# Performance work log

Hardware: AMD Instinct MI355X
Metric: run time of the kernel (lower is better)

The kernel has to match this reference:

```python
import jax, jax.numpy as jnp
import numpy as np

V, T, K, L, D = 256, 256, 36, 32, 1024
TAU = 0.05
MODE = 0
NEG_INF = -jnp.inf


def setup_inputs() -> dict:
    key = jax.random.key(0)
    k1, k2 = jax.random.split(key)
    imgs = jax.random.normal(k1, (V, K, D), dtype=jnp.float32)
    caps = jax.random.normal(k2, (T, L, D), dtype=jnp.float32)
    # Full lengths: the original module writes -inf into sim and 0 into w at
    # padded positions, so padding would produce -inf*0 = NaN in the output.
    img_lens = jnp.full((V,), K, dtype=jnp.int32)
    cap_lens = jnp.full((T,), L, dtype=jnp.int32)
    return {"imgs": imgs, "caps": caps, "img_lens": img_lens, "cap_lens": cap_lens}


def _l2norm(x):
    return x / jnp.maximum(jnp.linalg.norm(x, axis=-1, keepdims=True), 1e-12)


def reference(imgs, caps, img_lens, cap_lens):
    # masks: [V,K], [T,L]
    img_mask = (jnp.arange(K)[None, :] < img_lens[:, None]).astype(imgs.dtype)
    cap_mask = (jnp.arange(L)[None, :] < cap_lens[:, None]).astype(caps.dtype)
    # AvePool: masked mean over valid tokens, then L2-normalize
    img_glo = _l2norm((imgs * img_mask[:, :, None]).sum(1) / img_lens[:, None].astype(imgs.dtype))
    cap_glo = _l2norm((caps * cap_mask[:, :, None]).sum(1) / cap_lens[:, None].astype(caps.dtype))
    # ds: [V,T,K], et: [V,T,L]  (computed as in the original; note the original
    # forward overwrites w with the masked sim, so ds/et/softmax do not affect
    # the returned value — we keep only the live dataflow here)
    ds = jnp.einsum('vkd,td->vtk', imgs, cap_glo)
    et = jnp.einsum('tld,vd->vtl', caps, img_glo)
    del ds, et  # dead in the original (w is reassigned to masked sim)
    # sim: [V,T,K,L]
    sim = jnp.einsum('vkd,tld->vtkl', imgs, caps)
    sim_mask = img_mask[:, None, :, None] * cap_mask[None, :, None, :]  # [V,T,K,L]
    valid = sim_mask != 0
    sim = jnp.where(valid, sim, NEG_INF)
    # final w in the original is sim.masked_fill(sim_mask == 0, 0)
    w = jnp.where(valid, sim, 0.0)
    return jnp.einsum('vtkl,vtkl->vt', sim, w)
```

## Files before the change

### kernel.cpp

```cpp
#include <hip/hip_runtime.h>

#define V_N 256
#define T_N 256
#define K_N 36
#define L_N 32
#define D_N 1024
#define MROWS (V_N * K_N)
#define NROWS (T_N * L_N)
#define BM 256
#define BN 256
#define BK 64
#define KSTEPS (D_N / BK)
#define NBM (MROWS / BM)
#define NBN (NROWS / BN)
#define NWG (NBM * NBN)
#define NCB (NROWS / 16)
#define CB_STRIDE 16384
#define KT_STRIDE 1024
#define KS_STRIDE 512

typedef __attribute__((ext_vector_type(8))) short bf16x8;
typedef __attribute__((ext_vector_type(4))) float f32x4;

#define SB0 __builtin_amdgcn_sched_barrier(0)
#define BAR __builtin_amdgcn_s_barrier()

__device__ __forceinline__ ushort f2bf(float x) {
  union { float f; unsigned int u; } c; c.f = x;
  unsigned int r = c.u + 0x7FFFu + ((c.u >> 16) & 1u);
  return (ushort)(r >> 16);
}

__global__ void cvt_a(const float* __restrict__ imgs, ushort* __restrict__ aws) {
  const int AQ = MROWS * (D_N / 4);
  for (int q = blockIdx.x * blockDim.x + threadIdx.x; q < AQ;
       q += gridDim.x * blockDim.x) {
    float4 f = reinterpret_cast<const float4*>(imgs)[q];
    ushort4 u; u.x = f2bf(f.x); u.y = f2bf(f.y); u.z = f2bf(f.z); u.w = f2bf(f.w);
    reinterpret_cast<ushort4*>(aws)[q] = u;
  }
}

__global__ void cvt_b2(const float* __restrict__ caps, ushort* __restrict__ b2) {
  const int NH = NCB * KSTEPS * 2;
  int gid = blockIdx.x * blockDim.x + threadIdx.x;
  int h = gid >> 6;
  int lane = gid & 63;
  if (h >= NH) return;
  int c  = h >> 5;
  int kt = (h >> 1) & 15;
  int ks = h & 1;
  int col = c * 16 + (lane & 15);
  int k   = kt * 64 + ks * 32 + ((lane >> 4) << 3);
  const float4* s = reinterpret_cast<const float4*>(caps + (size_t)col * D_N + k);
  float4 f0 = s[0], f1 = s[1];
  union { ushort u[8]; int4 v4; } pk;
  pk.u[0] = f2bf(f0.x); pk.u[1] = f2bf(f0.y); pk.u[2] = f2bf(f0.z); pk.u[3] = f2bf(f0.w);
  pk.u[4] = f2bf(f1.x); pk.u[5] = f2bf(f1.y); pk.u[6] = f2bf(f1.z); pk.u[7] = f2bf(f1.w);
  *reinterpret_cast<int4*>(b2 + (size_t)h * 512 + lane * 8) = pk.v4;
}

__global__ __launch_bounds__(512, 2) void gemm2(
    const ushort* __restrict__ aws, const ushort* __restrict__ b2,
    float* __restrict__ out) {
  __shared__ ushort lds[2 * BM * BK];

  int orig = (int)blockIdx.x;
  int xcd = orig & 7;
  int idx = orig >> 3;
  const int bn = xcd * 4 + (idx & 3);
  const int bm = idx >> 2;
  const int row0 = bm * BM;
  const int col0 = bn * BN;

  const int tid  = (int)threadIdx.x;
  const int lane = tid & 63;
  const int wid  = tid >> 6;
  const int wr   = wid >> 2;
  const int wc   = wid & 3;

  const int kb  = (lane >> 4) << 4;

  auto stageA = [&](int kt) {
    ushort* bufA = lds + (kt & 1) * (BM * BK);
#pragma unroll
    for (int it = 0; it < 4; ++it) {
      int q = it * 512 + tid;
      int r = q >> 3;
      int sw = ((q & 7) << 4) ^ ((r & 7) << 4);
      const ushort* ga = aws + (size_t)(row0 + r) * D_N + kt * BK + (sw >> 1);
      __builtin_amdgcn_global_load_lds(
          (const __attribute__((address_space(1))) void*)ga,
          (__attribute__((address_space(3))) void*)(bufA + q * 8), 16, 0, 0);
    }
  };

  auto rdA = [&](const ushort* bufA, int m, int ks) -> bf16x8 {
    int r = wr * 128 + m * 16 + (lane & 15);
    int sw = (ks * 64 + kb) ^ ((r & 7) << 4);
    return *reinterpret_cast<const bf16x8*>(bufA + r * BK + (sw >> 1));
  };

  const ushort* bbase = b2 + (size_t)(bn * 16 + wc * 4) * CB_STRIDE + lane * 8;

  f32x4 acc[8][4];
#pragma unroll
  for (int m = 0; m < 8; ++m)
#pragma unroll
    for (int n = 0; n < 4; ++n) acc[m][n] = (f32x4){0.f, 0.f, 0.f, 0.f};

  stageA(0);
  stageA(1);
  asm volatile("s_waitcnt vmcnt(4)" ::: "memory");
  SB0; BAR; SB0;

  for (int t = 0; t < KSTEPS; ++t) {
    const ushort* bufA = lds + (t & 1) * (BM * BK);

    bf16x8 bfr[8];
#pragma unroll
    for (int n = 0; n < 4; ++n) {
      const ushort* bp = bbase + (size_t)n * CB_STRIDE + t * KT_STRIDE;
      bfr[n]     = *reinterpret_cast<const bf16x8*>(bp);
      bfr[4 + n] = *reinterpret_cast<const bf16x8*>(bp + KS_STRIDE);
    }

    bf16x8 aA0[8], aA1[8];
#pragma unroll
    for (int m = 0; m < 8; ++m) { aA0[m] = rdA(bufA, m, 0); aA1[m] = rdA(bufA, m, 1); }

    __builtin_amdgcn_s_setprio(1);
#pragma unroll
    for (int n = 0; n < 4; ++n)
#pragma unroll
      for (int m = 0; m < 8; ++m) {
        acc[m][n] = __builtin_amdgcn_mfma_f32_16x16x32_bf16(aA0[m], bfr[n], acc[m][n], 0, 0, 0);
        acc[m][n] = __builtin_amdgcn_mfma_f32_16x16x32_bf16(aA1[m], bfr[4 + n], acc[m][n], 0, 0, 0);
      }
    __builtin_amdgcn_s_setprio(0);

    if (t <= KSTEPS - 3) {
      SB0; BAR; SB0;
      stageA(t + 2);
      asm volatile("s_waitcnt vmcnt(4)" ::: "memory");
      SB0; BAR; SB0;
    } else if (t == KSTEPS - 2) {
      asm volatile("s_waitcnt vmcnt(0)" ::: "memory");
      SB0; BAR; SB0;
    }
  }

#pragma unroll
  for (int m = 0; m < 8; ++m) {
    int grow = row0 + wr * 128 + m * 16;
    int v0 = grow / K_N;
    int b = (v0 + 1) * K_N;
    int rb = grow + ((lane >> 4) << 2);
#pragma unroll
    for (int np = 0; np < 2; ++np) {
      float s0 = 0.f, s1 = 0.f;
#pragma unroll
      for (int nn = 0; nn < 2; ++nn) {
        f32x4 a4 = acc[m][np * 2 + nn];
#pragma unroll
        for (int rg = 0; rg < 4; ++rg) {
          float x = a4[rg];
          float x2 = x * x;
          if (rb + rg < b) s0 += x2; else s1 += x2;
        }
      }
#pragma unroll
      for (int off = 32; off > 0; off >>= 1) {
        s0 += __shfl_xor(s0, off, 64);
        s1 += __shfl_xor(s1, off, 64);
      }
      if (lane == 0) {
        int tcol = (col0 + wc * 64 + np * 32) >> 5;
        atomicAdd(out + v0 * T_N + tcol, s0);
        if (grow + 16 > b) atomicAdd(out + (v0 + 1) * T_N + tcol, s1);
      }
    }
  }
}

__global__ __launch_bounds__(256) void gemm_fb(
    const float* __restrict__ imgs, const float* __restrict__ caps,
    float* __restrict__ out) {
  __shared__ ushort lds[128 * 64 + 128 * 64];
  ushort* ldsA = lds;
  ushort* ldsB = lds + 128 * 64;
  const int NBMf = MROWS / 128, NBNf = NROWS / 128;
  int orig = (int)blockIdx.x;
  int xcd = orig & 7;
  int idx = orig >> 3;
  int bn = xcd * (NBNf / 8) + (idx % (NBNf / 8));
  int bm = idx / (NBNf / 8);
  const int row0 = bm * 128, col0 = bn * 128;
  const int tid = (int)threadIdx.x, lane = tid & 63, wid = tid >> 6;
  const int wr = wid >> 1, wc = wid & 1;
  f32x4 acc[4][4];
#pragma unroll
  for (int i = 0; i < 4; ++i)
#pragma unroll
    for (int j = 0; j < 4; ++j) acc[i][j] = (f32x4){0.f, 0.f, 0.f, 0.f};
  for (int kt = 0; kt < KSTEPS; ++kt) {
#pragma unroll
    for (int it = 0; it < 4; ++it) {
      int q = it * 256 + tid;
      int r = q >> 3;
      int sw = ((q & 7) << 4) ^ ((r & 7) << 4);
      const float4* src = reinterpret_cast<const float4*>(
          imgs + (size_t)(row0 + r) * D_N + kt * BK + (sw >> 1));
      float4 f0 = src[0], f1 = src[1];
      union { ushort u[8]; int4 v4; } pk;
      pk.u[0] = f2bf(f0.x); pk.u[1] = f2bf(f0.y); pk.u[2] = f2bf(f0.z); pk.u[3] = f2bf(f0.w);
      pk.u[4] = f2bf(f1.x); pk.u[5] = f2bf(f1.y); pk.u[6] = f2bf(f1.z); pk.u[7] = f2bf(f1.w);
      *reinterpret_cast<int4*>(ldsA + q * 8) = pk.v4;
    }
#pragma unroll
    for (int it = 0; it < 4; ++it) {
      int q = it * 256 + tid;
      int r = q >> 3;
      int sw = ((q & 7) << 4) ^ ((r & 7) << 4);
      const float4* src = reinterpret_cast<const float4*>(
          caps + (size_t)(col0 + r) * D_N + kt * BK + (sw >> 1));
      float4 f0 = src[0], f1 = src[1];
      union { ushort u[8]; int4 v4; } pk;
      pk.u[0] = f2bf(f0.x); pk.u[1] = f2bf(f0.y); pk.u[2] = f2bf(f0.z); pk.u[3] = f2bf(f0.w);
      pk.u[4] = f2bf(f1.x); pk.u[5] = f2bf(f1.y); pk.u[6] = f2bf(f1.z); pk.u[7] = f2bf(f1.w);
      *reinterpret_cast<int4*>(ldsB + q * 8) = pk.v4;
    }
    __syncthreads();
#pragma unroll
    for (int ks = 0; ks < 2; ++ks) {
      bf16x8 afr[4], bfr[4];
#pragma unroll
      for (int i = 0; i < 4; ++i) {
        int r = wr * 64 + i * 16 + (lane & 15);
        int sw = (ks * 64 + (((lane >> 4) << 4))) ^ ((r & 7) << 4);
        afr[i] = *reinterpret_cast<const bf16x8*>(ldsA + r * BK + (sw >> 1));
      }
#pragma unroll
      for (int j = 0; j < 4; ++j) {
        int r = wc * 64 + j * 16 + (lane & 15);
        int sw = (ks * 64 + (((lane >> 4) << 4))) ^ ((r & 7) << 4);
        bfr[j] = *reinterpret_cast<const bf16x8*>(ldsB + r * BK + (sw >> 1));
      }
#pragma unroll
      for (int i = 0; i < 4; ++i)
#pragma unroll
        for (int j = 0; j < 4; ++j)
          acc[i][j] = __builtin_amdgcn_mfma_f32_16x16x32_bf16(afr[i], bfr[j], acc[i][j], 0, 0, 0);
    }
    __syncthreads();
  }
#pragma unroll
  for (int i = 0; i < 4; ++i) {
#pragma unroll
    for (int j = 0; j < 4; ++j) {
      f32x4 a4 = acc[i][j];
      int grow = row0 + wr * 64 + i * 16;
      int gcol = col0 + wc * 64 + j * 16;
      int t = gcol >> 5;
      int v0 = grow / K_N;
      int b = (v0 + 1) * K_N;
      int rbase = grow + ((lane >> 4) << 2);
      float s0 = 0.f, s1 = 0.f;
#pragma unroll
      for (int rg = 0; rg < 4; ++rg) {
        float x = a4[rg];
        float x2 = x * x;
        if (rbase + rg < b) s0 += x2; else s1 += x2;
      }
#pragma unroll
      for (int off = 32; off > 0; off >>= 1) {
        s0 += __shfl_xor(s0, off, 64);
        s1 += __shfl_xor(s1, off, 64);
      }
      if (lane == 0) {
        atomicAdd(out + v0 * T_N + t, s0);
        if (b < grow + 16) atomicAdd(out + (v0 + 1) * T_N + t, s1);
      }
    }
  }
}

extern "C" void kernel_launch(void* const* d_in, const int* in_sizes, int n_in,
                              void* d_out, int out_size, void* d_ws, size_t ws_size,
                              hipStream_t stream) {
  const float* imgs = (const float*)d_in[0];
  const float* caps = (const float*)d_in[1];
  float* out = (float*)d_out;

  hipMemsetAsync(d_out, 0, (size_t)V_N * T_N * sizeof(float), stream);

  const size_t need = (size_t)(MROWS + NROWS) * D_N * sizeof(ushort);

  if (ws_size >= need) {
    ushort* aws = (ushort*)d_ws;
    ushort* b2  = aws + (size_t)MROWS * D_N;
    cvt_a<<<2048, 256, 0, stream>>>(imgs, aws);
    cvt_b2<<<(NCB * KSTEPS * 2 * 64) / 256, 256, 0, stream>>>(caps, b2);
    gemm2<<<NWG, 512, 0, stream>>>(aws, b2, out);
  } else {
    const int nwg = (MROWS / 128) * (NROWS / 128);
    gemm_fb<<<nwg, 256, 0, stream>>>(imgs, caps, out);
  }
}
```

Measured before the change: 200.6 us.

## Triple-buffer A tiles in LDS and prefetch half-step register fragments

Grows the LDS ring for A tiles from two to three buffers, so global-to-LDS staging runs two k-steps ahead. Each k-step is split into two halves: the A and B fragments for the second half are loaded while the first half's MFMAs run, and the next step's first-half fragments are loaded after the barrier. The aim is to hide LDS and global load latency behind MFMA work. The cost is more LDS per block (about 96 KB), which may not leave room for the two blocks per CU that the launch bounds request, plus more live fragment registers.

```diff
diff --git a/kernel.cpp b/kernel.cpp
--- a/kernel.cpp
+++ b/kernel.cpp
@@ -63,7 +63,7 @@
 __global__ __launch_bounds__(512, 2) void gemm2(
     const ushort* __restrict__ aws, const ushort* __restrict__ b2,
     float* __restrict__ out) {
-  __shared__ ushort lds[2 * BM * BK];
+  __shared__ ushort lds[3 * BM * BK];
 
   int orig = (int)blockIdx.x;
   int xcd = orig & 7;
@@ -82,7 +82,7 @@
   const int kb  = (lane >> 4) << 4;
 
   auto stageA = [&](int kt) {
-    ushort* bufA = lds + (kt & 1) * (BM * BK);
+    ushort* bufA = lds + (kt % 3) * (BM * BK);
 #pragma unroll
     for (int it = 0; it < 4; ++it) {
       int q = it * 512 + tid;
@@ -102,6 +102,10 @@
   };
 
   const ushort* bbase = b2 + (size_t)(bn * 16 + wc * 4) * CB_STRIDE + lane * 8;
+  auto ldB = [&](int t, int ks, int n) -> bf16x8 {
+    return *reinterpret_cast<const bf16x8*>(
+        bbase + (size_t)n * CB_STRIDE + t * KT_STRIDE + ks * KS_STRIDE);
+  };
 
   f32x4 acc[8][4];
 #pragma unroll
@@ -109,44 +113,60 @@
 #pragma unroll
     for (int n = 0; n < 4; ++n) acc[m][n] = (f32x4){0.f, 0.f, 0.f, 0.f};
 
-  stageA(0);
-  stageA(1);
-  asm volatile("s_waitcnt vmcnt(4)" ::: "memory");
+  bf16x8 regA0[8], regA1[8], regB0[4], regB1[4];
+
+  stageA(0); stageA(1); stageA(2);
+  SB0;
+  asm volatile("s_waitcnt vmcnt(8)" ::: "memory");
   SB0; BAR; SB0;
+#pragma unroll
+  for (int m = 0; m < 8; ++m) regA0[m] = rdA(lds, m, 0);
+  SB0;
+#pragma unroll
+  for (int n = 0; n < 4; ++n) regB0[n] = ldB(0, 0, n);
+  SB0;
 
   for (int t = 0; t < KSTEPS; ++t) {
-    const ushort* bufA = lds + (t & 1) * (BM * BK);
-
-    bf16x8 bfr[8];
-#pragma unroll
-    for (int n = 0; n < 4; ++n) {
-      const ushort* bp = bbase + (size_t)n * CB_STRIDE + t * KT_STRIDE;
-      bfr[n]     = *reinterpret_cast<const bf16x8*>(bp);
-      bfr[4 + n] = *reinterpret_cast<const bf16x8*>(bp + KS_STRIDE);
-    }
-
-    bf16x8 aA0[8], aA1[8];
-#pragma unroll
-    for (int m = 0; m < 8; ++m) { aA0[m] = rdA(bufA, m, 0); aA1[m] = rdA(bufA, m, 1); }
-
-    __builtin_amdgcn_s_setprio(1);
+    const ushort* bufA = lds + (t % 3) * (BM * BK);
+
+#pragma unroll
+    for (int m = 0; m < 8; ++m) regA1[m] = rdA(bufA, m, 1);
+    SB0;
+#pragma unroll
+    for (int n = 0; n < 4; ++n) regB1[n] = ldB(t, 1, n);
+    SB0;
+    asm volatile("s_waitcnt lgkmcnt(8)" ::: "memory");
+    SB0;
 #pragma unroll
     for (int n = 0; n < 4; ++n)
 #pragma unroll
-      for (int m = 0; m < 8; ++m) {
-        acc[m][n] = __builtin_amdgcn_mfma_f32_16x16x32_bf16(aA0[m], bfr[n], acc[m][n], 0, 0, 0);
-        acc[m][n] = __builtin_amdgcn_mfma_f32_16x16x32_bf16(aA1[m], bfr[4 + n], acc[m][n], 0, 0, 0);
-      }
-    __builtin_amdgcn_s_setprio(0);
-
-    if (t <= KSTEPS - 3) {
+      for (int m = 0; m < 8; ++m)
+        acc[m][n] = __builtin_amdgcn_mfma_f32_16x16x32_bf16(regA0[m], regB0[n], acc[m][n], 0, 0, 0);
+    SB0;
+
+    asm volatile("s_waitcnt lgkmcnt(0)" ::: "memory");
+    SB0;
+#pragma unroll
+    for (int n = 0; n < 4; ++n)
+#pragma unroll
+      for (int m = 0; m < 8; ++m)
+        acc[m][n] = __builtin_amdgcn_mfma_f32_16x16x32_bf16(regA1[m], regB1[n], acc[m][n], 0, 0, 0);
+    SB0;
+
+    if (t < KSTEPS - 1) {
+      BAR; SB0;
+      if (t <= KSTEPS - 4) { stageA(t + 3); SB0; }
+      if (t <= KSTEPS - 4)      { asm volatile("s_waitcnt vmcnt(8)" ::: "memory"); }
+      else if (t == KSTEPS - 3) { asm volatile("s_waitcnt vmcnt(4)" ::: "memory"); }
+      else                      { asm volatile("s_waitcnt vmcnt(0)" ::: "memory"); }
       SB0; BAR; SB0;
-      stageA(t + 2);
-      asm volatile("s_waitcnt vmcnt(4)" ::: "memory");
-      SB0; BAR; SB0;
-    } else if (t == KSTEPS - 2) {
-      asm volatile("s_waitcnt vmcnt(0)" ::: "memory");
-      SB0; BAR; SB0;
+      const ushort* bufN = lds + ((t + 1) % 3) * (BM * BK);
+#pragma unroll
+      for (int m = 0; m < 8; ++m) regA0[m] = rdA(bufN, m, 0);
+      SB0;
+#pragma unroll
+      for (int n = 0; n < 4; ++n) regB0[n] = ldB(t + 1, 0, n);
+      SB0;
     }
   }
 
```

New measurement: 199.9 us. Within noise of the previous version (-0.4%).

## Switch GEMM to 128x128 tiles with 32x32x16 MFMA and repacked B layout

Applied to the files above, without the earlier changes.

Replaces the 256x256-tile, 512-thread GEMM built on 16x16x32 MFMAs with a 128x128-tile, 256-thread kernel using 32x32x16 bf16 MFMAs. The B pre-pack is reorganised to match the 32-column fragment layout, and the epilogue row mapping is updated for the 32x32 accumulator layout. A-tile staging is reduced to a single-step prefetch with a full vmcnt(0) wait and barrier every iteration. The aim is higher occupancy (3 blocks per CU) and fewer, larger MFMA instructions, at the cost of less data reuse per tile and a shallower pipeline.

```diff
diff --git a/kernel.cpp b/kernel.cpp
--- a/kernel.cpp
+++ b/kernel.cpp
@@ -7,20 +7,17 @@
 #define D_N 1024
 #define MROWS (V_N * K_N)
 #define NROWS (T_N * L_N)
-#define BM 256
-#define BN 256
+#define BM 128
+#define BN 128
 #define BK 64
 #define KSTEPS (D_N / BK)
 #define NBM (MROWS / BM)
 #define NBN (NROWS / BN)
 #define NWG (NBM * NBN)
-#define NCB (NROWS / 16)
-#define CB_STRIDE 16384
-#define KT_STRIDE 1024
-#define KS_STRIDE 512
 
 typedef __attribute__((ext_vector_type(8))) short bf16x8;
 typedef __attribute__((ext_vector_type(4))) float f32x4;
+typedef __attribute__((ext_vector_type(16))) float f32x16;
 
 #define SB0 __builtin_amdgcn_sched_barrier(0)
 #define BAR __builtin_amdgcn_s_barrier()
@@ -42,25 +39,24 @@
 }
 
 __global__ void cvt_b2(const float* __restrict__ caps, ushort* __restrict__ b2) {
-  const int NH = NCB * KSTEPS * 2;
+  const int NH = 256 * 64;
   int gid = blockIdx.x * blockDim.x + threadIdx.x;
   int h = gid >> 6;
   int lane = gid & 63;
   if (h >= NH) return;
-  int c  = h >> 5;
-  int kt = (h >> 1) & 15;
-  int ks = h & 1;
-  int col = c * 16 + (lane & 15);
-  int k   = kt * 64 + ks * 32 + ((lane >> 4) << 3);
-  const float4* s = reinterpret_cast<const float4*>(caps + (size_t)col * D_N + k);
-  float4 f0 = s[0], f1 = s[1];
+  int c = h >> 6;
+  int s = h & 63;
+  int col = c * 32 + (lane & 31);
+  int k   = s * 16 + ((lane >> 5) << 3);
+  const float4* src = reinterpret_cast<const float4*>(caps + (size_t)col * D_N + k);
+  float4 f0 = src[0], f1 = src[1];
   union { ushort u[8]; int4 v4; } pk;
   pk.u[0] = f2bf(f0.x); pk.u[1] = f2bf(f0.y); pk.u[2] = f2bf(f0.z); pk.u[3] = f2bf(f0.w);
   pk.u[4] = f2bf(f1.x); pk.u[5] = f2bf(f1.y); pk.u[6] = f2bf(f1.z); pk.u[7] = f2bf(f1.w);
   *reinterpret_cast<int4*>(b2 + (size_t)h * 512 + lane * 8) = pk.v4;
 }
 
-__global__ __launch_bounds__(512, 2) void gemm2(
+__global__ __launch_bounds__(256, 3) void gemm3(
     const ushort* __restrict__ aws, const ushort* __restrict__ b2,
     float* __restrict__ out) {
   __shared__ ushort lds[2 * BM * BK];
@@ -68,106 +64,100 @@
   int orig = (int)blockIdx.x;
   int xcd = orig & 7;
   int idx = orig >> 3;
-  const int bn = xcd * 4 + (idx & 3);
-  const int bm = idx >> 2;
+  const int bn = xcd * 8 + (idx & 7);
+  const int bm = idx >> 3;
   const int row0 = bm * BM;
   const int col0 = bn * BN;
 
   const int tid  = (int)threadIdx.x;
   const int lane = tid & 63;
   const int wid  = tid >> 6;
-  const int wr   = wid >> 2;
-  const int wc   = wid & 3;
-
-  const int kb  = (lane >> 4) << 4;
+  const int wr   = wid >> 1;
+  const int wc   = wid & 1;
 
   auto stageA = [&](int kt) {
-    ushort* bufA = lds + (kt & 1) * (BM * BK);
+    ushort* buf = lds + (kt & 1) * (BM * BK);
 #pragma unroll
     for (int it = 0; it < 4; ++it) {
-      int q = it * 512 + tid;
+      int q = it * 256 + tid;
       int r = q >> 3;
       int sw = ((q & 7) << 4) ^ ((r & 7) << 4);
       const ushort* ga = aws + (size_t)(row0 + r) * D_N + kt * BK + (sw >> 1);
       __builtin_amdgcn_global_load_lds(
           (const __attribute__((address_space(1))) void*)ga,
-          (__attribute__((address_space(3))) void*)(bufA + q * 8), 16, 0, 0);
+          (__attribute__((address_space(3))) void*)(buf + q * 8), 16, 0, 0);
     }
   };
 
-  auto rdA = [&](const ushort* bufA, int m, int ks) -> bf16x8 {
-    int r = wr * 128 + m * 16 + (lane & 15);
-    int sw = (ks * 64 + kb) ^ ((r & 7) << 4);
-    return *reinterpret_cast<const bf16x8*>(bufA + r * BK + (sw >> 1));
+  auto rdA = [&](const ushort* buf, int mt, int ks) -> bf16x8 {
+    int r = wr * 64 + mt * 32 + (lane & 31);
+    int cb = ks * 32 + ((lane >> 5) << 4);
+    int sw = cb ^ ((r & 7) << 4);
+    return *reinterpret_cast<const bf16x8*>(buf + r * 64 + (sw >> 1));
   };
 
-  const ushort* bbase = b2 + (size_t)(bn * 16 + wc * 4) * CB_STRIDE + lane * 8;
-
-  f32x4 acc[8][4];
-#pragma unroll
-  for (int m = 0; m < 8; ++m)
-#pragma unroll
-    for (int n = 0; n < 4; ++n) acc[m][n] = (f32x4){0.f, 0.f, 0.f, 0.f};
+  const ushort* bbase = b2 + ((size_t)(bn * 4 + wc * 2) * 64) * 512 + lane * 8;
+  auto ldB = [&](int t, int nt, int ks) -> bf16x8 {
+    return *reinterpret_cast<const bf16x8*>(
+        bbase + ((size_t)nt * 64 + t * 4 + ks) * 512);
+  };
+
+  f32x16 acc[2][2];
+#pragma unroll
+  for (int mt = 0; mt < 2; ++mt)
+#pragma unroll
+    for (int nt = 0; nt < 2; ++nt)
+#pragma unroll
+      for (int j = 0; j < 16; ++j) acc[mt][nt][j] = 0.f;
 
   stageA(0);
-  stageA(1);
-  asm volatile("s_waitcnt vmcnt(4)" ::: "memory");
+  asm volatile("s_waitcnt vmcnt(0)" ::: "memory");
   SB0; BAR; SB0;
 
   for (int t = 0; t < KSTEPS; ++t) {
-    const ushort* bufA = lds + (t & 1) * (BM * BK);
-
-    bf16x8 bfr[8];
-#pragma unroll
-    for (int n = 0; n < 4; ++n) {
-      const ushort* bp = bbase + (size_t)n * CB_STRIDE + t * KT_STRIDE;
-      bfr[n]     = *reinterpret_cast<const bf16x8*>(bp);
-      bfr[4 + n] = *reinterpret_cast<const bf16x8*>(bp + KS_STRIDE);
-    }
-
-    bf16x8 aA0[8], aA1[8];
-#pragma unroll
-    for (int m = 0; m < 8; ++m) { aA0[m] = rdA(bufA, m, 0); aA1[m] = rdA(bufA, m, 1); }
-
-    __builtin_amdgcn_s_setprio(1);
-#pragma unroll
-    for (int n = 0; n < 4; ++n)
-#pragma unroll
-      for (int m = 0; m < 8; ++m) {
-        acc[m][n] = __builtin_amdgcn_mfma_f32_16x16x32_bf16(aA0[m], bfr[n], acc[m][n], 0, 0, 0);
-        acc[m][n] = __builtin_amdgcn_mfma_f32_16x16x32_bf16(aA1[m], bfr[4 + n], acc[m][n], 0, 0, 0);
-      }
-    __builtin_amdgcn_s_setprio(0);
-
-    if (t <= KSTEPS - 3) {
-      SB0; BAR; SB0;
-      stageA(t + 2);
-      asm volatile("s_waitcnt vmcnt(4)" ::: "memory");
-      SB0; BAR; SB0;
-    } else if (t == KSTEPS - 2) {
-      asm volatile("s_waitcnt vmcnt(0)" ::: "memory");
-      SB0; BAR; SB0;
-    }
-  }
-
-#pragma unroll
-  for (int m = 0; m < 8; ++m) {
-    int grow = row0 + wr * 128 + m * 16;
-    int v0 = grow / K_N;
+    const ushort* buf = lds + (t & 1) * (BM * BK);
+    if (t < KSTEPS - 1) stageA(t + 1);
+
+    bf16x8 bB[8], aA[8];
+#pragma unroll
+    for (int ks = 0; ks < 4; ++ks) {
+      bB[ks * 2]     = ldB(t, 0, ks);
+      bB[ks * 2 + 1] = ldB(t, 1, ks);
+    }
+#pragma unroll
+    for (int ks = 0; ks < 4; ++ks) {
+      aA[ks * 2]     = rdA(buf, 0, ks);
+      aA[ks * 2 + 1] = rdA(buf, 1, ks);
+    }
+
+#pragma unroll
+    for (int ks = 0; ks < 4; ++ks)
+#pragma unroll
+      for (int mt = 0; mt < 2; ++mt)
+#pragma unroll
+        for (int nt = 0; nt < 2; ++nt)
+          acc[mt][nt] = __builtin_amdgcn_mfma_f32_32x32x16_bf16(
+              aA[ks * 2 + mt], bB[ks * 2 + nt], acc[mt][nt], 0, 0, 0);
+
+    asm volatile("s_waitcnt vmcnt(0)" ::: "memory");
+    SB0; BAR; SB0;
+  }
+
+#pragma unroll
+  for (int mt = 0; mt < 2; ++mt) {
+    int gbase = row0 + wr * 64 + mt * 32;
+    int v0 = gbase / K_N;
     int b = (v0 + 1) * K_N;
-    int rb = grow + ((lane >> 4) << 2);
-#pragma unroll
-    for (int np = 0; np < 2; ++np) {
+#pragma unroll
+    for (int nt = 0; nt < 2; ++nt) {
+      f32x16 a = acc[mt][nt];
       float s0 = 0.f, s1 = 0.f;
 #pragma unroll
-      for (int nn = 0; nn < 2; ++nn) {
-        f32x4 a4 = acc[m][np * 2 + nn];
-#pragma unroll
-        for (int rg = 0; rg < 4; ++rg) {
-          float x = a4[rg];
-          float x2 = x * x;
-          if (rb + rg < b) s0 += x2; else s1 += x2;
-        }
+      for (int j = 0; j < 16; ++j) {
+        int row = (j & 3) + 8 * (j >> 2) + 4 * (lane >> 5);
+        float x = a[j];
+        float x2 = x * x;
+        if (gbase + row < b) s0 += x2; else s1 += x2;
       }
 #pragma unroll
       for (int off = 32; off > 0; off >>= 1) {
@@ -175,9 +165,9 @@
         s1 += __shfl_xor(s1, off, 64);
       }
       if (lane == 0) {
-        int tcol = (col0 + wc * 64 + np * 32) >> 5;
+        int tcol = (col0 + wc * 64 + nt * 32) >> 5;
         atomicAdd(out + v0 * T_N + tcol, s0);
-        if (grow + 16 > b) atomicAdd(out + (v0 + 1) * T_N + tcol, s1);
+        if (b < gbase + 32) atomicAdd(out + (v0 + 1) * T_N + tcol, s1);
       }
     }
   }
@@ -300,8 +290,8 @@
     ushort* aws = (ushort*)d_ws;
     ushort* b2  = aws + (size_t)MROWS * D_N;
     cvt_a<<<2048, 256, 0, stream>>>(imgs, aws);
-    cvt_b2<<<(NCB * KSTEPS * 2 * 64) / 256, 256, 0, stream>>>(caps, b2);
-    gemm2<<<NWG, 512, 0, stream>>>(aws, b2, out);
+    cvt_b2<<<4096, 256, 0, stream>>>(caps, b2);
+    gemm3<<<NWG, 256, 0, stream>>>(aws, b2, out);
   } else {
     const int nwg = (MROWS / 128) * (NROWS / 128);
     gemm_fb<<<nwg, 256, 0, stream>>>(imgs, caps, out);
```

Result: faster. 189.8 us (-5.4%).
